# Kernel tuning notes

Measured on AMD Instinct MI355X. Metric: run time of the kernel, lower is better.

## Reference

```python
import jax, jax.numpy as jnp
import numpy as np
from jax import lax

B = 64
N_WIRES = 4
NUM_CENTERS = 64


def setup_inputs() -> dict:
    key = jax.random.key(0)
    ks = jax.random.split(key, 17)
    f32 = jnp.float32

    def w(k, shape, fan_in):
        return jax.random.normal(k, shape, dtype=f32) * (1.0 / np.sqrt(fan_in))

    return {
        "x": jax.random.normal(ks[0], (B, 3, 250, 250), dtype=f32),
        # conv backbone
        "conv1_w": w(ks[1], (6, 3, 5, 5), 3 * 25),
        "conv1_b": jnp.zeros((6,), f32),
        "conv2_w": w(ks[2], (15, 6, 3, 3), 6 * 9),
        "conv2_b": jnp.zeros((15,), f32),
        # MLP head of feature extractor
        "fc1_w": w(ks[3], (120, 55815), 55815),
        "fc1_b": jnp.zeros((120,), f32),
        "fc2_w": w(ks[4], (84, 120), 120),
        "fc2_b": jnp.zeros((84,), f32),
        # quantum kernel centers (num_centers, input_dim=84)
        "centers": jax.random.normal(ks[5], (NUM_CENTERS, 84), dtype=f32),
        # classifier: depth=2 hidden layers of width num_centers, then head->2
        "cls_w1": w(ks[6], (NUM_CENTERS, NUM_CENTERS), NUM_CENTERS),
        "cls_b1": jnp.zeros((NUM_CENTERS,), f32),
        "cls_w2": w(ks[7], (NUM_CENTERS, NUM_CENTERS), NUM_CENTERS),
        "cls_b2": jnp.zeros((NUM_CENTERS,), f32),
        "cls_w3": w(ks[8], (2, NUM_CENTERS), NUM_CENTERS),
        "cls_b3": jnp.zeros((2,), f32),
    }


def _maxpool2_s1(h):
    # MaxPool2d(kernel_size=2, stride=1), VALID padding
    return lax.reduce_window(h, -jnp.inf, lax.max, (1, 1, 2, 2), (1, 1, 1, 1), "VALID")


def reference(x, conv1_w, conv1_b, conv2_w, conv2_b, fc1_w, fc1_b, fc2_w, fc2_b,
              centers, cls_w1, cls_b1, cls_w2, cls_b2, cls_w3, cls_b3):
    dn = ("NCHW", "OIHW", "NCHW")
    # Conv(3->6, k5, s2, p1) + ReLU + MaxPool(2, s1)   (dropout = identity in eval)
    h = lax.conv_general_dilated(x, conv1_w, (2, 2), [(1, 1), (1, 1)], dimension_numbers=dn)
    h = jax.nn.relu(h + conv1_b[None, :, None, None])
    h = _maxpool2_s1(h)                                   # [B,6,123,123]
    # Conv(6->15, k3, s2, p1) + ReLU + MaxPool(2, s1)
    h = lax.conv_general_dilated(h, conv2_w, (2, 2), [(1, 1), (1, 1)], dimension_numbers=dn)
    h = jax.nn.relu(h + conv2_b[None, :, None, None])
    h = _maxpool2_s1(h)                                   # [B,15,61,61]
    h = h.reshape(h.shape[0], -1)                         # [B,55815]
    h = jax.nn.relu(h @ fc1_w.T + fc1_b)                  # [B,120]
    feat = jax.nn.relu(h @ fc2_w.T + fc2_b)               # [B,84]

    # Quantum fidelity kernel over n_wires=4 qubits:
    # encode RY(x_i) then RY(-c_i) per wire on |0>, read |0...0| amplitude ->
    # k[b,c] = |prod_i cos((x_i - c_i)/2)| over the first 4 feature dims.
    diff = feat[:, None, :N_WIRES] - centers[None, :, :N_WIRES]  # [B,C,4]
    k = jnp.abs(jnp.prod(jnp.cos(0.5 * diff), axis=-1))          # [B,C]

    h = jax.nn.relu(k @ cls_w1.T + cls_b1)
    h = jax.nn.relu(h @ cls_w2.T + cls_b2)
    logits = h @ cls_w3.T + cls_b3                        # [B,2]
    return jax.nn.softmax(logits, axis=-1)
```

## Files before the change

kernel.cpp:

```cpp
#include <hip/hip_runtime.h>
#include <hip/hip_bf16.h>

typedef float float4a __attribute__((ext_vector_type(4), aligned(4)));
typedef float float2a __attribute__((ext_vector_type(2), aligned(4)));
typedef short bfrag   __attribute__((ext_vector_type(8)));
typedef float f32x4   __attribute__((ext_vector_type(4)));

#define P1W_PAD 128
#define APAD 56064
#define KFC 55815
#define CHUNK 256
#define NCHUNK 219
#define NFC1 120

#define oP1B   ((size_t)0)
#define oAB    ((size_t)24182784)
#define oPARTB ((size_t)38535168)

__global__ __launch_bounds__(256) void conv1_pool(const float* __restrict__ x,
        const float* __restrict__ w, const float* __restrict__ bias,
        float* __restrict__ p1) {
    __shared__ float ex[8 * 6 * 128];
    const int tid = threadIdx.x;
    const int G = blockIdx.x;
    const int b = blockIdx.y;
    const int t = tid >> 5;
    const int s = tid & 31;
    const int r = 7 * G + t;
    const bool act = (r < 124) && (s < 31);

    if (act) {
        float acc[6][4];
        #pragma unroll
        for (int c = 0; c < 6; ++c) {
            const float bz = bias[c];
            #pragma unroll
            for (int j = 0; j < 4; ++j) acc[c][j] = bz;
        }
        for (int ic = 0; ic < 3; ++ic) {
            const float* xpl = x + (size_t)(b * 3 + ic) * 62500;
            #pragma unroll
            for (int ky = 0; ky < 5; ++ky) {
                const int iy = 2 * r - 1 + ky;
                if (iy < 0) continue;
                const float* rp = xpl + iy * 250 + 8 * s;
                float a[11];
                a[0] = (s > 0) ? rp[-1] : 0.f;
                *(float4a*)&a[1] = *(const float4a*)rp;
                *(float4a*)&a[5] = *(const float4a*)(rp + 4);
                *(float2a*)&a[9] = *(const float2a*)(rp + 8);
                const float* wb = w + ic * 25 + ky * 5;
                #pragma unroll
                for (int c = 0; c < 6; ++c) {
                    #pragma unroll
                    for (int kx = 0; kx < 5; ++kx) {
                        const float wv = wb[c * 75 + kx];
                        #pragma unroll
                        for (int j = 0; j < 4; ++j)
                            acc[c][j] = fmaf(a[2 * j + kx], wv, acc[c][j]);
                    }
                }
            }
        }
        #pragma unroll
        for (int c = 0; c < 6; ++c)
            *(float4*)&ex[(t * 6 + c) * 128 + 4 * s] = *(float4*)&acc[c][0];
    }
    __syncthreads();
    const int np = min(7, 123 - 7 * G);
    for (int idx = tid; idx < np * 768; idx += 256) {
        const int p   = idx / 768;
        const int rem = idx - p * 768;
        const int c   = rem >> 7;
        const int pc  = rem & 127;
        float v = 0.f;
        if (pc < 123) {
            const float* r0 = &ex[((p    ) * 6 + c) * 128 + pc];
            const float* r1 = &ex[((p + 1) * 6 + c) * 128 + pc];
            v = fmaxf(fmaxf(fmaxf(r0[0], r0[1]), fmaxf(r1[0], r1[1])), 0.f);
        }
        p1[((size_t)(b * 6 + c) * 123 + (7 * G + p)) * P1W_PAD + pc] = v;
    }
}

__global__ __launch_bounds__(256) void conv2_pool(const float* __restrict__ p1,
        const float* __restrict__ w, const float* __restrict__ bias,
        float* __restrict__ A) {
    __shared__ float ex[16 * 5 * 64];
    const int tid = threadIdx.x;
    const int G = blockIdx.x;
    const int b = blockIdx.y;
    const int cb = blockIdx.z * 5;
    const int t = tid >> 4;
    const int s = tid & 15;
    const int r = 15 * G + t;
    const bool act = (r < 62);

    if (act) {
        float acc[5][4];
        #pragma unroll
        for (int c = 0; c < 5; ++c) {
            const float bz = bias[cb + c];
            #pragma unroll
            for (int j = 0; j < 4; ++j) acc[c][j] = bz;
        }
        for (int ic = 0; ic < 6; ++ic) {
            const float* pl = p1 + (size_t)(b * 6 + ic) * 123 * P1W_PAD;
            #pragma unroll
            for (int ky = 0; ky < 3; ++ky) {
                const int iy = 2 * r - 1 + ky;
                if (iy < 0 || iy > 122) continue;
                const float* rp = pl + iy * P1W_PAD + 8 * s;
                float a[9];
                a[0] = (s > 0) ? rp[-1] : 0.f;
                *(float4a*)&a[1] = *(const float4a*)rp;
                *(float4a*)&a[5] = *(const float4a*)(rp + 4);
                const float* wb = w + ic * 9 + ky * 3;
                #pragma unroll
                for (int c = 0; c < 5; ++c) {
                    #pragma unroll
                    for (int kx = 0; kx < 3; ++kx) {
                        const float wv = wb[(cb + c) * 54 + kx];
                        #pragma unroll
                        for (int j = 0; j < 4; ++j)
                            acc[c][j] = fmaf(a[2 * j + kx], wv, acc[c][j]);
                    }
                }
            }
        }
        #pragma unroll
        for (int c = 0; c < 5; ++c)
            *(float4*)&ex[(t * 5 + c) * 64 + 4 * s] = *(float4*)&acc[c][0];
    }
    __syncthreads();
    const int np = min(15, 61 - 15 * G);
    for (int idx = tid; idx < np * 305; idx += 256) {
        const int p   = idx / 305;
        const int rem = idx % 305;
        const int c   = rem / 61;
        const int pc  = rem % 61;
        const float* r0 = &ex[((p    ) * 5 + c) * 64 + pc];
        const float* r1 = &ex[((p + 1) * 5 + c) * 64 + pc];
        const float v = fmaxf(fmaxf(r0[0], r0[1]), fmaxf(r1[0], r1[1]));
        A[(size_t)b * APAD + (cb + c) * 3721 + (15 * G + p) * 61 + pc] = fmaxf(v, 0.f);
    }
    if (G == 0 && cb == 0)
        for (int i2 = tid; i2 < 249; i2 += 256)
            A[(size_t)b * APAD + KFC + i2] = 0.f;
}

__global__ __launch_bounds__(256) void fc1_s1(const float* __restrict__ A,
        const float* __restrict__ W, float* __restrict__ part) {
    const int cBlk = blockIdx.x;
    const int nth  = blockIdx.y;
    const int k0 = cBlk * CHUNK;
    const int tid = threadIdx.x;
    const int lane  = tid & 63;
    const int mtile = tid >> 6;
    const int ocol  = lane & 15;
    const int kq    = lane >> 4;
    const int arow  = mtile * 16 + ocol;

    const float* ab = A + (size_t)arow * APAD + k0 + kq * 8;
    const float* wb[2];
    #pragma unroll
    for (int ntl = 0; ntl < 2; ++ntl) {
        const int o = (nth * 2 + ntl) * 16 + ocol;
        wb[ntl] = W + (size_t)min(o, NFC1 - 1) * KFC + k0 + kq * 8;
    }

    f32x4 acc[2];
    #pragma unroll
    for (int n = 0; n < 2; ++n) acc[n] = (f32x4){0.f, 0.f, 0.f, 0.f};

    const bool full = (cBlk != NCHUNK - 1);
    #pragma unroll 2
    for (int ks = 0; ks < 8; ++ks) {
        float af[8];
        *(float4a*)&af[0] = *(const float4a*)(ab + ks * 32);
        *(float4a*)&af[4] = *(const float4a*)(ab + ks * 32 + 4);
        bfrag ah, al;
        #pragma unroll
        for (int e = 0; e < 8; ++e) {
            const unsigned u = __float_as_uint(af[e]);
            ah[e] = (short)(u >> 16);
            const float rres = af[e] - __uint_as_float(u & 0xffff0000u);
            al[e] = (short)(__float_as_uint(rres) >> 16);
        }
        #pragma unroll
        for (int ntl = 0; ntl < 2; ++ntl) {
            float wf[8];
            if (full) {
                *(float4a*)&wf[0] = *(const float4a*)(wb[ntl] + ks * 32);
                *(float4a*)&wf[4] = *(const float4a*)(wb[ntl] + ks * 32 + 4);
            } else {
                const int kg = k0 + ks * 32 + kq * 8;
                #pragma unroll
                for (int e = 0; e < 8; ++e)
                    wf[e] = (kg + e < KFC) ? wb[ntl][ks * 32 + e] : 0.f;
            }
            bfrag wh, wl;
            #pragma unroll
            for (int e = 0; e < 8; ++e) {
                const unsigned u = __float_as_uint(wf[e]);
                wh[e] = (short)(u >> 16);
                const float rres = wf[e] - __uint_as_float(u & 0xffff0000u);
                wl[e] = (short)(__float_as_uint(rres) >> 16);
            }
            acc[ntl] = __builtin_amdgcn_mfma_f32_16x16x32_bf16(ah, wh, acc[ntl], 0, 0, 0);
            acc[ntl] = __builtin_amdgcn_mfma_f32_16x16x32_bf16(al, wh, acc[ntl], 0, 0, 0);
            acc[ntl] = __builtin_amdgcn_mfma_f32_16x16x32_bf16(ah, wl, acc[ntl], 0, 0, 0);
        }
    }
    #pragma unroll
    for (int ntl = 0; ntl < 2; ++ntl) {
        const int o = (nth * 2 + ntl) * 16 + ocol;
        if (o < NFC1) {
            #pragma unroll
            for (int rr = 0; rr < 4; ++rr) {
                const int brow = mtile * 16 + kq * 4 + rr;
                part[((size_t)cBlk * 64 + brow) * NFC1 + o] = acc[ntl][rr];
            }
        }
    }
}

__global__ __launch_bounds__(1024) void tail_k(const float* __restrict__ part,
        const float* __restrict__ fc1b,
        const float* __restrict__ fc2w, const float* __restrict__ fc2b,
        const float* __restrict__ centers,
        const float* __restrict__ w1, const float* __restrict__ b1,
        const float* __restrict__ w2, const float* __restrict__ b2,
        const float* __restrict__ w3, const float* __restrict__ b3,
        float* __restrict__ out) {
    const int b = blockIdx.x;
    const int tid = threadIdx.x;
    __shared__ float partial[960];
    __shared__ float h[120];
    __shared__ float feat[4];
    __shared__ float bufA[64];
    __shared__ float bufB[64];

    if (tid < 960) {
        const int o = tid % 120;
        const int g = tid / 120;
        const int c0 = g * 27 + min(g, 3);
        const int n  = 27 + (g < 3 ? 1 : 0);
        float s0 = 0.f, s1 = 0.f, s2 = 0.f, s3 = 0.f;
        int c = c0;
        for (; c + 3 < c0 + n; c += 4) {
            s0 += part[((size_t)(c + 0) * 64 + b) * NFC1 + o];
            s1 += part[((size_t)(c + 1) * 64 + b) * NFC1 + o];
            s2 += part[((size_t)(c + 2) * 64 + b) * NFC1 + o];
            s3 += part[((size_t)(c + 3) * 64 + b) * NFC1 + o];
        }
        for (; c < c0 + n; ++c) s0 += part[((size_t)c * 64 + b) * NFC1 + o];
        partial[g * 120 + o] = (s0 + s1) + (s2 + s3);
    }
    __syncthreads();
    if (tid < 120) {
        float sv = fc1b[tid];
        #pragma unroll
        for (int g = 0; g < 8; ++g) sv += partial[g * 120 + tid];
        h[tid] = fmaxf(sv, 0.f);
    }
    __syncthreads();

    if (tid < 64) {
        const int j = tid >> 4, p = tid & 15;
        float sv = 0.f;
        for (int o = p; o < NFC1; o += 16) sv = fmaf(fc2w[j * NFC1 + o], h[o], sv);
        #pragma unroll
        for (int off = 8; off; off >>= 1) sv += __shfl_xor(sv, off, 16);
        if (p == 0) feat[j] = fmaxf(sv + fc2b[j], 0.f);
    }
    __syncthreads();

    if (tid < 64) {
        float prod = 1.f;
        #pragma unroll
        for (int i = 0; i < 4; ++i) prod *= cosf(0.5f * (feat[i] - centers[tid * 84 + i]));
        bufA[tid] = fabsf(prod);
    }
    __syncthreads();
    if (tid < 64) {
        float s1v = b1[tid];
        for (int jj = 0; jj < 64; ++jj) s1v = fmaf(w1[tid * 64 + jj], bufA[jj], s1v);
        bufB[tid] = fmaxf(s1v, 0.f);
    }
    __syncthreads();
    if (tid < 64) {
        float s2v = b2[tid];
        for (int jj = 0; jj < 64; ++jj) s2v = fmaf(w2[tid * 64 + jj], bufB[jj], s2v);
        bufA[tid] = fmaxf(s2v, 0.f);
    }
    __syncthreads();
    if (tid < 2) {
        float s3v = b3[tid];
        for (int jj = 0; jj < 64; ++jj) s3v = fmaf(w3[tid * 64 + jj], bufA[jj], s3v);
        const float other = __shfl_xor(s3v, 1, 2);
        const float m = fmaxf(s3v, other);
        const float e = expf(s3v - m), eo = expf(other - m);
        out[b * 2 + tid] = e / (e + eo);
    }
}

extern "C" void kernel_launch(void* const* d_in, const int* in_sizes, int n_in,
                              void* d_out, int out_size, void* d_ws, size_t ws_size,
                              hipStream_t stream) {
    const float* x       = (const float*)d_in[0];
    const float* conv1_w = (const float*)d_in[1];
    const float* conv1_b = (const float*)d_in[2];
    const float* conv2_w = (const float*)d_in[3];
    const float* conv2_b = (const float*)d_in[4];
    const float* fc1_w   = (const float*)d_in[5];
    const float* fc1_b   = (const float*)d_in[6];
    const float* fc2_w   = (const float*)d_in[7];
    const float* fc2_b   = (const float*)d_in[8];
    const float* centers = (const float*)d_in[9];
    const float* cls_w1  = (const float*)d_in[10];
    const float* cls_b1  = (const float*)d_in[11];
    const float* cls_w2  = (const float*)d_in[12];
    const float* cls_b2  = (const float*)d_in[13];
    const float* cls_w3  = (const float*)d_in[14];
    const float* cls_b3  = (const float*)d_in[15];
    char* ws = (char*)d_ws;
    float* outp = (float*)d_out;

    float* p1    = (float*)(ws + oP1B);
    float* Abuf  = (float*)(ws + oAB);
    float* partb = (float*)(ws + oPARTB);

    hipLaunchKernelGGL(conv1_pool, dim3(18, 64), dim3(256), 0, stream, x, conv1_w, conv1_b, p1);
    hipLaunchKernelGGL(conv2_pool, dim3(5, 64, 3), dim3(256), 0, stream, p1, conv2_w, conv2_b, Abuf);
    hipLaunchKernelGGL(fc1_s1, dim3(NCHUNK, 4), dim3(256), 0, stream, Abuf, fc1_w, partb);
    hipLaunchKernelGGL(tail_k, dim3(64), dim3(1024), 0, stream,
                       partb, fc1_b, fc2_w, fc2_b, centers,
                       cls_w1, cls_b1, cls_w2, cls_b2, cls_w3, cls_b3, outp);
}
```

Before: 77.19 us.

## Fuse all four stages into one cooperative persistent kernel with grid syncs

Replaces the four separate launches (conv1+pool, conv2+pool, fc1 partials, tail) with a single cooperative kernel of 256 blocks × 1024 threads. Each block runs four 256-thread teams that each play the role of one former block, and grid-wide syncs separate the stages. This removes the inter-kernel launch gaps and drain bubbles. In exchange, each block has a single 1024-thread workgroup with about 96KB of shared memory, which limits occupancy. Conv1 now needs two rounds per team, the grid syncs add their own cost, and every thread in a 1024-thread block waits on the per-team __syncthreads.

```diff
diff --git a/kernel.cpp b/kernel.cpp
--- a/kernel.cpp
+++ b/kernel.cpp
@@ -1,5 +1,8 @@
 #include <hip/hip_runtime.h>
 #include <hip/hip_bf16.h>
+#include <hip/hip_cooperative_groups.h>
+
+namespace cg = cooperative_groups;
 
 typedef float float4a __attribute__((ext_vector_type(4), aligned(4)));
 typedef float float2a __attribute__((ext_vector_type(2), aligned(4)));
@@ -17,291 +20,311 @@
 #define oAB    ((size_t)24182784)
 #define oPARTB ((size_t)38535168)
 
-__global__ __launch_bounds__(256) void conv1_pool(const float* __restrict__ x,
-        const float* __restrict__ w, const float* __restrict__ bias,
-        float* __restrict__ p1) {
-    __shared__ float ex[8 * 6 * 128];
-    const int tid = threadIdx.x;
-    const int G = blockIdx.x;
-    const int b = blockIdx.y;
-    const int t = tid >> 5;
-    const int s = tid & 31;
-    const int r = 7 * G + t;
-    const bool act = (r < 124) && (s < 31);
-
-    if (act) {
-        float acc[6][4];
-        #pragma unroll
-        for (int c = 0; c < 6; ++c) {
-            const float bz = bias[c];
-            #pragma unroll
-            for (int j = 0; j < 4; ++j) acc[c][j] = bz;
-        }
-        for (int ic = 0; ic < 3; ++ic) {
-            const float* xpl = x + (size_t)(b * 3 + ic) * 62500;
-            #pragma unroll
-            for (int ky = 0; ky < 5; ++ky) {
-                const int iy = 2 * r - 1 + ky;
-                if (iy < 0) continue;
-                const float* rp = xpl + iy * 250 + 8 * s;
-                float a[11];
-                a[0] = (s > 0) ? rp[-1] : 0.f;
-                *(float4a*)&a[1] = *(const float4a*)rp;
-                *(float4a*)&a[5] = *(const float4a*)(rp + 4);
-                *(float2a*)&a[9] = *(const float2a*)(rp + 8);
-                const float* wb = w + ic * 25 + ky * 5;
-                #pragma unroll
-                for (int c = 0; c < 6; ++c) {
-                    #pragma unroll
-                    for (int kx = 0; kx < 5; ++kx) {
-                        const float wv = wb[c * 75 + kx];
-                        #pragma unroll
-                        for (int j = 0; j < 4; ++j)
-                            acc[c][j] = fmaf(a[2 * j + kx], wv, acc[c][j]);
-                    }
-                }
-            }
-        }
-        #pragma unroll
-        for (int c = 0; c < 6; ++c)
-            *(float4*)&ex[(t * 6 + c) * 128 + 4 * s] = *(float4*)&acc[c][0];
-    }
-    __syncthreads();
-    const int np = min(7, 123 - 7 * G);
-    for (int idx = tid; idx < np * 768; idx += 256) {
-        const int p   = idx / 768;
-        const int rem = idx - p * 768;
-        const int c   = rem >> 7;
-        const int pc  = rem & 127;
-        float v = 0.f;
-        if (pc < 123) {
-            const float* r0 = &ex[((p    ) * 6 + c) * 128 + pc];
-            const float* r1 = &ex[((p + 1) * 6 + c) * 128 + pc];
-            v = fmaxf(fmaxf(fmaxf(r0[0], r0[1]), fmaxf(r1[0], r1[1])), 0.f);
-        }
-        p1[((size_t)(b * 6 + c) * 123 + (7 * G + p)) * P1W_PAD + pc] = v;
-    }
-}
-
-__global__ __launch_bounds__(256) void conv2_pool(const float* __restrict__ p1,
-        const float* __restrict__ w, const float* __restrict__ bias,
-        float* __restrict__ A) {
-    __shared__ float ex[16 * 5 * 64];
-    const int tid = threadIdx.x;
-    const int G = blockIdx.x;
-    const int b = blockIdx.y;
-    const int cb = blockIdx.z * 5;
-    const int t = tid >> 4;
-    const int s = tid & 15;
-    const int r = 15 * G + t;
-    const bool act = (r < 62);
-
-    if (act) {
-        float acc[5][4];
-        #pragma unroll
-        for (int c = 0; c < 5; ++c) {
-            const float bz = bias[cb + c];
-            #pragma unroll
-            for (int j = 0; j < 4; ++j) acc[c][j] = bz;
-        }
-        for (int ic = 0; ic < 6; ++ic) {
-            const float* pl = p1 + (size_t)(b * 6 + ic) * 123 * P1W_PAD;
-            #pragma unroll
-            for (int ky = 0; ky < 3; ++ky) {
-                const int iy = 2 * r - 1 + ky;
-                if (iy < 0 || iy > 122) continue;
-                const float* rp = pl + iy * P1W_PAD + 8 * s;
-                float a[9];
-                a[0] = (s > 0) ? rp[-1] : 0.f;
-                *(float4a*)&a[1] = *(const float4a*)rp;
-                *(float4a*)&a[5] = *(const float4a*)(rp + 4);
-                const float* wb = w + ic * 9 + ky * 3;
-                #pragma unroll
-                for (int c = 0; c < 5; ++c) {
-                    #pragma unroll
-                    for (int kx = 0; kx < 3; ++kx) {
-                        const float wv = wb[(cb + c) * 54 + kx];
-                        #pragma unroll
-                        for (int j = 0; j < 4; ++j)
-                            acc[c][j] = fmaf(a[2 * j + kx], wv, acc[c][j]);
-                    }
-                }
-            }
-        }
-        #pragma unroll
-        for (int c = 0; c < 5; ++c)
-            *(float4*)&ex[(t * 5 + c) * 64 + 4 * s] = *(float4*)&acc[c][0];
-    }
-    __syncthreads();
-    const int np = min(15, 61 - 15 * G);
-    for (int idx = tid; idx < np * 305; idx += 256) {
-        const int p   = idx / 305;
-        const int rem = idx % 305;
-        const int c   = rem / 61;
-        const int pc  = rem % 61;
-        const float* r0 = &ex[((p    ) * 5 + c) * 64 + pc];
-        const float* r1 = &ex[((p + 1) * 5 + c) * 64 + pc];
-        const float v = fmaxf(fmaxf(r0[0], r0[1]), fmaxf(r1[0], r1[1]));
-        A[(size_t)b * APAD + (cb + c) * 3721 + (15 * G + p) * 61 + pc] = fmaxf(v, 0.f);
-    }
-    if (G == 0 && cb == 0)
-        for (int i2 = tid; i2 < 249; i2 += 256)
-            A[(size_t)b * APAD + KFC + i2] = 0.f;
-}
-
-__global__ __launch_bounds__(256) void fc1_s1(const float* __restrict__ A,
-        const float* __restrict__ W, float* __restrict__ part) {
-    const int cBlk = blockIdx.x;
-    const int nth  = blockIdx.y;
-    const int k0 = cBlk * CHUNK;
-    const int tid = threadIdx.x;
-    const int lane  = tid & 63;
-    const int mtile = tid >> 6;
-    const int ocol  = lane & 15;
-    const int kq    = lane >> 4;
-    const int arow  = mtile * 16 + ocol;
-
-    const float* ab = A + (size_t)arow * APAD + k0 + kq * 8;
-    const float* wb[2];
-    #pragma unroll
-    for (int ntl = 0; ntl < 2; ++ntl) {
-        const int o = (nth * 2 + ntl) * 16 + ocol;
-        wb[ntl] = W + (size_t)min(o, NFC1 - 1) * KFC + k0 + kq * 8;
-    }
-
-    f32x4 acc[2];
-    #pragma unroll
-    for (int n = 0; n < 2; ++n) acc[n] = (f32x4){0.f, 0.f, 0.f, 0.f};
-
-    const bool full = (cBlk != NCHUNK - 1);
-    #pragma unroll 2
-    for (int ks = 0; ks < 8; ++ks) {
-        float af[8];
-        *(float4a*)&af[0] = *(const float4a*)(ab + ks * 32);
-        *(float4a*)&af[4] = *(const float4a*)(ab + ks * 32 + 4);
-        bfrag ah, al;
-        #pragma unroll
-        for (int e = 0; e < 8; ++e) {
-            const unsigned u = __float_as_uint(af[e]);
-            ah[e] = (short)(u >> 16);
-            const float rres = af[e] - __uint_as_float(u & 0xffff0000u);
-            al[e] = (short)(__float_as_uint(rres) >> 16);
-        }
-        #pragma unroll
-        for (int ntl = 0; ntl < 2; ++ntl) {
-            float wf[8];
-            if (full) {
-                *(float4a*)&wf[0] = *(const float4a*)(wb[ntl] + ks * 32);
-                *(float4a*)&wf[4] = *(const float4a*)(wb[ntl] + ks * 32 + 4);
-            } else {
-                const int kg = k0 + ks * 32 + kq * 8;
-                #pragma unroll
-                for (int e = 0; e < 8; ++e)
-                    wf[e] = (kg + e < KFC) ? wb[ntl][ks * 32 + e] : 0.f;
-            }
-            bfrag wh, wl;
-            #pragma unroll
-            for (int e = 0; e < 8; ++e) {
-                const unsigned u = __float_as_uint(wf[e]);
-                wh[e] = (short)(u >> 16);
-                const float rres = wf[e] - __uint_as_float(u & 0xffff0000u);
-                wl[e] = (short)(__float_as_uint(rres) >> 16);
-            }
-            acc[ntl] = __builtin_amdgcn_mfma_f32_16x16x32_bf16(ah, wh, acc[ntl], 0, 0, 0);
-            acc[ntl] = __builtin_amdgcn_mfma_f32_16x16x32_bf16(al, wh, acc[ntl], 0, 0, 0);
-            acc[ntl] = __builtin_amdgcn_mfma_f32_16x16x32_bf16(ah, wl, acc[ntl], 0, 0, 0);
-        }
-    }
-    #pragma unroll
-    for (int ntl = 0; ntl < 2; ++ntl) {
-        const int o = (nth * 2 + ntl) * 16 + ocol;
-        if (o < NFC1) {
-            #pragma unroll
-            for (int rr = 0; rr < 4; ++rr) {
-                const int brow = mtile * 16 + kq * 4 + rr;
-                part[((size_t)cBlk * 64 + brow) * NFC1 + o] = acc[ntl][rr];
-            }
-        }
-    }
-}
-
-__global__ __launch_bounds__(1024) void tail_k(const float* __restrict__ part,
-        const float* __restrict__ fc1b,
+__global__ __launch_bounds__(1024) void fused_all(
+        const float* __restrict__ x,
+        const float* __restrict__ c1w, const float* __restrict__ c1b,
+        const float* __restrict__ c2w, const float* __restrict__ c2b,
+        const float* __restrict__ W,   const float* __restrict__ fc1b,
         const float* __restrict__ fc2w, const float* __restrict__ fc2b,
         const float* __restrict__ centers,
         const float* __restrict__ w1, const float* __restrict__ b1,
         const float* __restrict__ w2, const float* __restrict__ b2,
         const float* __restrict__ w3, const float* __restrict__ b3,
-        float* __restrict__ out) {
-    const int b = blockIdx.x;
-    const int tid = threadIdx.x;
-    __shared__ float partial[960];
-    __shared__ float h[120];
-    __shared__ float feat[4];
-    __shared__ float bufA[64];
-    __shared__ float bufB[64];
-
-    if (tid < 960) {
-        const int o = tid % 120;
-        const int g = tid / 120;
-        const int c0 = g * 27 + min(g, 3);
-        const int n  = 27 + (g < 3 ? 1 : 0);
-        float s0 = 0.f, s1 = 0.f, s2 = 0.f, s3 = 0.f;
-        int c = c0;
-        for (; c + 3 < c0 + n; c += 4) {
-            s0 += part[((size_t)(c + 0) * 64 + b) * NFC1 + o];
-            s1 += part[((size_t)(c + 1) * 64 + b) * NFC1 + o];
-            s2 += part[((size_t)(c + 2) * 64 + b) * NFC1 + o];
-            s3 += part[((size_t)(c + 3) * 64 + b) * NFC1 + o];
-        }
-        for (; c < c0 + n; ++c) s0 += part[((size_t)c * 64 + b) * NFC1 + o];
-        partial[g * 120 + o] = (s0 + s1) + (s2 + s3);
+        float* __restrict__ p1, float* __restrict__ A,
+        float* __restrict__ part, float* __restrict__ out) {
+    cg::grid_group gg = cg::this_grid();
+    __shared__ float smem[4 * 6144];
+    const int bid  = blockIdx.x;
+    const int tid  = threadIdx.x;
+    const int team = tid >> 8;
+    const int lt   = tid & 255;
+    float* tsm = smem + team * 6144;
+
+    for (int rnd = 0; rnd < 2; ++rnd) {
+        const int u = rnd * 1024 + bid * 4 + team;
+        const bool uok = (u < 1152);
+        const int G = uok ? (u % 18) : 0;
+        const int b = uok ? (u / 18) : 0;
+        const int t = lt >> 5;
+        const int s = lt & 31;
+        const int r = 7 * G + t;
+        const bool act = uok && (r < 124) && (s < 31);
+
+        if (act) {
+            float acc[6][4];
+            #pragma unroll
+            for (int c = 0; c < 6; ++c) {
+                const float bz = c1b[c];
+                #pragma unroll
+                for (int j = 0; j < 4; ++j) acc[c][j] = bz;
+            }
+            for (int ic = 0; ic < 3; ++ic) {
+                const float* xpl = x + (size_t)(b * 3 + ic) * 62500;
+                #pragma unroll
+                for (int ky = 0; ky < 5; ++ky) {
+                    const int iy = 2 * r - 1 + ky;
+                    if (iy < 0) continue;
+                    const float* rp = xpl + iy * 250 + 8 * s;
+                    float a[11];
+                    a[0] = (s > 0) ? rp[-1] : 0.f;
+                    *(float4a*)&a[1] = *(const float4a*)rp;
+                    *(float4a*)&a[5] = *(const float4a*)(rp + 4);
+                    *(float2a*)&a[9] = *(const float2a*)(rp + 8);
+                    const float* wb = c1w + ic * 25 + ky * 5;
+                    #pragma unroll
+                    for (int c = 0; c < 6; ++c) {
+                        #pragma unroll
+                        for (int kx = 0; kx < 5; ++kx) {
+                            const float wv = wb[c * 75 + kx];
+                            #pragma unroll
+                            for (int j = 0; j < 4; ++j)
+                                acc[c][j] = fmaf(a[2 * j + kx], wv, acc[c][j]);
+                        }
+                    }
+                }
+            }
+            #pragma unroll
+            for (int c = 0; c < 6; ++c)
+                *(float4*)&tsm[(t * 6 + c) * 128 + 4 * s] = *(float4*)&acc[c][0];
+        }
+        __syncthreads();
+        if (uok) {
+            const int np = min(7, 123 - 7 * G);
+            for (int idx = lt; idx < np * 768; idx += 256) {
+                const int p   = idx / 768;
+                const int rem = idx - p * 768;
+                const int c   = rem >> 7;
+                const int pc  = rem & 127;
+                float v = 0.f;
+                if (pc < 123) {
+                    const float* r0 = &tsm[((p    ) * 6 + c) * 128 + pc];
+                    const float* r1 = &tsm[((p + 1) * 6 + c) * 128 + pc];
+                    v = fmaxf(fmaxf(fmaxf(r0[0], r0[1]), fmaxf(r1[0], r1[1])), 0.f);
+                }
+                p1[((size_t)(b * 6 + c) * 123 + (7 * G + p)) * P1W_PAD + pc] = v;
+            }
+        }
+        __syncthreads();
     }
-    __syncthreads();
-    if (tid < 120) {
-        float sv = fc1b[tid];
-        #pragma unroll
-        for (int g = 0; g < 8; ++g) sv += partial[g * 120 + tid];
-        h[tid] = fmaxf(sv, 0.f);
+    gg.sync();
+
+    {
+        const int u = bid * 4 + team;
+        const bool uok = (u < 960);
+        const int G  = uok ? (u % 5) : 0;
+        const int b  = uok ? ((u / 5) % 64) : 0;
+        const int cb = uok ? ((u / 320) * 5) : 0;
+        const int t = lt >> 4;
+        const int s = lt & 15;
+        const int r = 15 * G + t;
+        const bool act = uok && (r < 62);
+
+        if (act) {
+            float acc[5][4];
+            #pragma unroll
+            for (int c = 0; c < 5; ++c) {
+                const float bz = c2b[cb + c];
+                #pragma unroll
+                for (int j = 0; j < 4; ++j) acc[c][j] = bz;
+            }
+            for (int ic = 0; ic < 6; ++ic) {
+                const float* pl = p1 + (size_t)(b * 6 + ic) * 123 * P1W_PAD;
+                #pragma unroll
+                for (int ky = 0; ky < 3; ++ky) {
+                    const int iy = 2 * r - 1 + ky;
+                    if (iy < 0 || iy > 122) continue;
+                    const float* rp = pl + iy * P1W_PAD + 8 * s;
+                    float a[9];
+                    a[0] = (s > 0) ? rp[-1] : 0.f;
+                    *(float4a*)&a[1] = *(const float4a*)rp;
+                    *(float4a*)&a[5] = *(const float4a*)(rp + 4);
+                    const float* wb = c2w + ic * 9 + ky * 3;
+                    #pragma unroll
+                    for (int c = 0; c < 5; ++c) {
+                        #pragma unroll
+                        for (int kx = 0; kx < 3; ++kx) {
+                            const float wv = wb[(cb + c) * 54 + kx];
+                            #pragma unroll
+                            for (int j = 0; j < 4; ++j)
+                                acc[c][j] = fmaf(a[2 * j + kx], wv, acc[c][j]);
+                        }
+                    }
+                }
+            }
+            #pragma unroll
+            for (int c = 0; c < 5; ++c)
+                *(float4*)&tsm[(t * 5 + c) * 64 + 4 * s] = *(float4*)&acc[c][0];
+        }
+        __syncthreads();
+        if (uok) {
+            const int np = min(15, 61 - 15 * G);
+            for (int idx = lt; idx < np * 305; idx += 256) {
+                const int p   = idx / 305;
+                const int rem = idx % 305;
+                const int c   = rem / 61;
+                const int pc  = rem % 61;
+                const float* r0 = &tsm[((p    ) * 5 + c) * 64 + pc];
+                const float* r1 = &tsm[((p + 1) * 5 + c) * 64 + pc];
+                const float v = fmaxf(fmaxf(r0[0], r0[1]), fmaxf(r1[0], r1[1]));
+                A[(size_t)b * APAD + (cb + c) * 3721 + (15 * G + p) * 61 + pc] = fmaxf(v, 0.f);
+            }
+            if (G == 0 && cb == 0)
+                for (int i2 = lt; i2 < 249; i2 += 256)
+                    A[(size_t)b * APAD + KFC + i2] = 0.f;
+        }
+        __syncthreads();
     }
-    __syncthreads();
-
-    if (tid < 64) {
-        const int j = tid >> 4, p = tid & 15;
-        float sv = 0.f;
-        for (int o = p; o < NFC1; o += 16) sv = fmaf(fc2w[j * NFC1 + o], h[o], sv);
-        #pragma unroll
-        for (int off = 8; off; off >>= 1) sv += __shfl_xor(sv, off, 16);
-        if (p == 0) feat[j] = fmaxf(sv + fc2b[j], 0.f);
+    gg.sync();
+
+    {
+        const int u = bid * 4 + team;
+        if (u < 876) {
+            const int cBlk = u % 219;
+            const int nth  = u / 219;
+            const int k0 = cBlk * CHUNK;
+            const int lane  = lt & 63;
+            const int mtile = lt >> 6;
+            const int ocol  = lane & 15;
+            const int kq    = lane >> 4;
+            const int arow  = mtile * 16 + ocol;
+
+            const float* ab = A + (size_t)arow * APAD + k0 + kq * 8;
+            const float* wbp[2];
+            #pragma unroll
+            for (int ntl = 0; ntl < 2; ++ntl) {
+                const int o = (nth * 2 + ntl) * 16 + ocol;
+                wbp[ntl] = W + (size_t)min(o, NFC1 - 1) * KFC + k0 + kq * 8;
+            }
+
+            f32x4 acc[2];
+            #pragma unroll
+            for (int n = 0; n < 2; ++n) acc[n] = (f32x4){0.f, 0.f, 0.f, 0.f};
+
+            const bool full = (cBlk != NCHUNK - 1);
+            #pragma unroll 2
+            for (int ks = 0; ks < 8; ++ks) {
+                float af[8];
+                *(float4a*)&af[0] = *(const float4a*)(ab + ks * 32);
+                *(float4a*)&af[4] = *(const float4a*)(ab + ks * 32 + 4);
+                bfrag ah, al;
+                #pragma unroll
+                for (int e = 0; e < 8; ++e) {
+                    const unsigned uu = __float_as_uint(af[e]);
+                    ah[e] = (short)(uu >> 16);
+                    const float rres = af[e] - __uint_as_float(uu & 0xffff0000u);
+                    al[e] = (short)(__float_as_uint(rres) >> 16);
+                }
+                #pragma unroll
+                for (int ntl = 0; ntl < 2; ++ntl) {
+                    float wf[8];
+                    if (full) {
+                        *(float4a*)&wf[0] = *(const float4a*)(wbp[ntl] + ks * 32);
+                        *(float4a*)&wf[4] = *(const float4a*)(wbp[ntl] + ks * 32 + 4);
+                    } else {
+                        const int kg = k0 + ks * 32 + kq * 8;
+                        #pragma unroll
+                        for (int e = 0; e < 8; ++e)
+                            wf[e] = (kg + e < KFC) ? wbp[ntl][ks * 32 + e] : 0.f;
+                    }
+                    bfrag wh, wl;
+                    #pragma unroll
+                    for (int e = 0; e < 8; ++e) {
+                        const unsigned uu = __float_as_uint(wf[e]);
+                        wh[e] = (short)(uu >> 16);
+                        const float rres = wf[e] - __uint_as_float(uu & 0xffff0000u);
+                        wl[e] = (short)(__float_as_uint(rres) >> 16);
+                    }
+                    acc[ntl] = __builtin_amdgcn_mfma_f32_16x16x32_bf16(ah, wh, acc[ntl], 0, 0, 0);
+                    acc[ntl] = __builtin_amdgcn_mfma_f32_16x16x32_bf16(al, wh, acc[ntl], 0, 0, 0);
+                    acc[ntl] = __builtin_amdgcn_mfma_f32_16x16x32_bf16(ah, wl, acc[ntl], 0, 0, 0);
+                }
+            }
+            #pragma unroll
+            for (int ntl = 0; ntl < 2; ++ntl) {
+                const int o = (nth * 2 + ntl) * 16 + ocol;
+                if (o < NFC1) {
+                    #pragma unroll
+                    for (int rr = 0; rr < 4; ++rr) {
+                        const int brow = mtile * 16 + kq * 4 + rr;
+                        part[((size_t)cBlk * 64 + brow) * NFC1 + o] = acc[ntl][rr];
+                    }
+                }
+            }
+        }
     }
-    __syncthreads();
-
-    if (tid < 64) {
-        float prod = 1.f;
-        #pragma unroll
-        for (int i = 0; i < 4; ++i) prod *= cosf(0.5f * (feat[i] - centers[tid * 84 + i]));
-        bufA[tid] = fabsf(prod);
-    }
-    __syncthreads();
-    if (tid < 64) {
-        float s1v = b1[tid];
-        for (int jj = 0; jj < 64; ++jj) s1v = fmaf(w1[tid * 64 + jj], bufA[jj], s1v);
-        bufB[tid] = fmaxf(s1v, 0.f);
-    }
-    __syncthreads();
-    if (tid < 64) {
-        float s2v = b2[tid];
-        for (int jj = 0; jj < 64; ++jj) s2v = fmaf(w2[tid * 64 + jj], bufB[jj], s2v);
-        bufA[tid] = fmaxf(s2v, 0.f);
-    }
-    __syncthreads();
-    if (tid < 2) {
-        float s3v = b3[tid];
-        for (int jj = 0; jj < 64; ++jj) s3v = fmaf(w3[tid * 64 + jj], bufA[jj], s3v);
-        const float other = __shfl_xor(s3v, 1, 2);
-        const float m = fmaxf(s3v, other);
-        const float e = expf(s3v - m), eo = expf(other - m);
-        out[b * 2 + tid] = e / (e + eo);
+    gg.sync();
+
+    if (bid >= 64) return;
+    {
+        const int b = bid;
+        float* partial = smem;
+        float* h    = smem + 960;
+        float* feat = smem + 1080;
+        float* bufA = smem + 1084;
+        float* bufB = smem + 1148;
+
+        if (tid < 960) {
+            const int o = tid % 120;
+            const int g = tid / 120;
+            const int c0 = g * 27 + min(g, 3);
+            const int n  = 27 + (g < 3 ? 1 : 0);
+            float s0 = 0.f, s1v = 0.f, s2v = 0.f, s3v = 0.f;
+            int c = c0;
+            for (; c + 3 < c0 + n; c += 4) {
+                s0  += part[((size_t)(c + 0) * 64 + b) * NFC1 + o];
+                s1v += part[((size_t)(c + 1) * 64 + b) * NFC1 + o];
+                s2v += part[((size_t)(c + 2) * 64 + b) * NFC1 + o];
+                s3v += part[((size_t)(c + 3) * 64 + b) * NFC1 + o];
+            }
+            for (; c < c0 + n; ++c) s0 += part[((size_t)c * 64 + b) * NFC1 + o];
+            partial[g * 120 + o] = (s0 + s1v) + (s2v + s3v);
+        }
+        __syncthreads();
+        if (tid < 120) {
+            float sv = fc1b[tid];
+            #pragma unroll
+            for (int g = 0; g < 8; ++g) sv += partial[g * 120 + tid];
+            h[tid] = fmaxf(sv, 0.f);
+        }
+        __syncthreads();
+
+        if (tid < 64) {
+            const int j = tid >> 4, p = tid & 15;
+            float sv = 0.f;
+            for (int o = p; o < NFC1; o += 16) sv = fmaf(fc2w[j * NFC1 + o], h[o], sv);
+            #pragma unroll
+            for (int off = 8; off; off >>= 1) sv += __shfl_xor(sv, off, 16);
+            if (p == 0) feat[j] = fmaxf(sv + fc2b[j], 0.f);
+        }
+        __syncthreads();
+
+        if (tid < 64) {
+            float prod = 1.f;
+            #pragma unroll
+            for (int i = 0; i < 4; ++i) prod *= cosf(0.5f * (feat[i] - centers[tid * 84 + i]));
+            bufA[tid] = fabsf(prod);
+        }
+        __syncthreads();
+        if (tid < 64) {
+            float s1v = b1[tid];
+            for (int jj = 0; jj < 64; ++jj) s1v = fmaf(w1[tid * 64 + jj], bufA[jj], s1v);
+            bufB[tid] = fmaxf(s1v, 0.f);
+        }
+        __syncthreads();
+        if (tid < 64) {
+            float s2v = b2[tid];
+            for (int jj = 0; jj < 64; ++jj) s2v = fmaf(w2[tid * 64 + jj], bufB[jj], s2v);
+            bufA[tid] = fmaxf(s2v, 0.f);
+        }
+        __syncthreads();
+        if (tid < 2) {
+            float s3v = b3[tid];
+            for (int jj = 0; jj < 64; ++jj) s3v = fmaf(w3[tid * 64 + jj], bufA[jj], s3v);
+            const float other = __shfl_xor(s3v, 1, 2);
+            const float m = fmaxf(s3v, other);
+            const float e = expf(s3v - m), eo = expf(other - m);
+            out[b * 2 + tid] = e / (e + eo);
+        }
     }
 }
 
@@ -331,10 +354,12 @@
     float* Abuf  = (float*)(ws + oAB);
     float* partb = (float*)(ws + oPARTB);
 
-    hipLaunchKernelGGL(conv1_pool, dim3(18, 64), dim3(256), 0, stream, x, conv1_w, conv1_b, p1);
-    hipLaunchKernelGGL(conv2_pool, dim3(5, 64, 3), dim3(256), 0, stream, p1, conv2_w, conv2_b, Abuf);
-    hipLaunchKernelGGL(fc1_s1, dim3(NCHUNK, 4), dim3(256), 0, stream, Abuf, fc1_w, partb);
-    hipLaunchKernelGGL(tail_k, dim3(64), dim3(1024), 0, stream,
-                       partb, fc1_b, fc2_w, fc2_b, centers,
-                       cls_w1, cls_b1, cls_w2, cls_b2, cls_w3, cls_b3, outp);
+    void* args[] = {
+        (void*)&x, (void*)&conv1_w, (void*)&conv1_b, (void*)&conv2_w, (void*)&conv2_b,
+        (void*)&fc1_w, (void*)&fc1_b, (void*)&fc2_w, (void*)&fc2_b, (void*)&centers,
+        (void*)&cls_w1, (void*)&cls_b1, (void*)&cls_w2, (void*)&cls_b2,
+        (void*)&cls_w3, (void*)&cls_b3,
+        (void*)&p1, (void*)&Abuf, (void*)&partb, (void*)&outp
+    };
+    hipLaunchCooperativeKernel((void*)fused_all, dim3(256), dim3(1024), args, 0, stream);
 }
```

Result: slower. 193.9 us (+151.2%).
